# Performance work log

Hardware: AMD Instinct MI355X
Metric: run time of the kernel (lower is better)

## Reference

```python
import jax, jax.numpy as jnp
import numpy as np

COMMITMENT_COST = 0.25


def setup_inputs() -> dict:
    key = jax.random.key(0)
    k1, k2 = jax.random.split(key)
    B, S, D, K = 8, 4096, 256, 1024
    inputs = jax.random.normal(k1, (B, S, D), dtype=jnp.float32)
    attention_mask = jnp.ones((B, S), dtype=jnp.float32)
    codebook = jax.random.normal(k2, (K, D), dtype=jnp.float32)
    return {"inputs": inputs, "attention_mask": attention_mask, "codebook": codebook}


def reference(inputs, attention_mask, codebook):
    # Inference-mode forward of VectorQuantizer (no EMA update / init / revival).
    B, S, D = inputs.shape
    z = inputs.astype(jnp.float32).reshape(-1, D)          # (N, D)
    m = attention_mask.reshape(-1).astype(jnp.float32)     # (N,)

    cb = codebook.astype(jnp.float32)                      # (K, D)
    # squared L2 distances: ||z||^2 - 2 z e^T + ||e||^2
    dist = (jnp.sum(z * z, axis=-1, keepdims=True)
            - 2.0 * jnp.matmul(z, cb.T)
            + jnp.sum(cb * cb, axis=-1)[None, :])          # (N, K)
    idx = jnp.argmin(dist, axis=-1)                        # (N,)
    q = cb[idx]                                            # (N, D) codebook lookup

    n_valid = jnp.sum(m)
    # mse over valid tokens (elementwise mean, matching F.mse_loss on flat_valid)
    diff = z - jax.lax.stop_gradient(q)
    commitment = jnp.sum(m[:, None] * diff * diff) / (n_valid * D)
    vq_loss = COMMITMENT_COST * commitment

    # straight-through estimator; invalid positions zeroed (as in torch scatter)
    q_ste = z + jax.lax.stop_gradient(q - z)
    quantized = (q_ste * m[:, None]).reshape(B, S, D)
    indices = jnp.where(m > 0, idx, 0).reshape(B, S)
    return quantized, vq_loss, indices
```

## Files before the change

kernel.cpp:

```cpp
#include <hip/hip_runtime.h>
#include <cstdint>

typedef short bf16x8 __attribute__((ext_vector_type(8)));
typedef float f32x4  __attribute__((ext_vector_type(4)));

#define TOK    64
#define CH     64
#define NCH    16
#define BUFW   16384
#define MAXC   32

__device__ __forceinline__ unsigned short f2bf(float f) {
  unsigned u = __float_as_uint(f);
  return (unsigned short)((u + 0x7FFFu + ((u >> 16) & 1u)) >> 16);
}
__device__ __forceinline__ uint4 pack8(float4 a, float4 b) {
  uint4 u;
  u.x = (unsigned)f2bf(a.x) | ((unsigned)f2bf(a.y) << 16);
  u.y = (unsigned)f2bf(a.z) | ((unsigned)f2bf(a.w) << 16);
  u.z = (unsigned)f2bf(b.x) | ((unsigned)f2bf(b.y) << 16);
  u.w = (unsigned)f2bf(b.z) | ((unsigned)f2bf(b.w) << 16);
  return u;
}
__device__ __forceinline__ void gload16(const unsigned short* g, unsigned short* l) {
  __builtin_amdgcn_global_load_lds(
      (const __attribute__((address_space(1))) unsigned int*)(const void*)g,
      (__attribute__((address_space(3))) unsigned int*)(void*)l, 16, 0, 0);
}

__global__ __launch_bounds__(256) void vq_prep(const float* __restrict__ cb,
                                               unsigned short* __restrict__ cb_bf,
                                               float* __restrict__ ee,
                                               float* __restrict__ acc2,
                                               int* __restrict__ done_ctr, int K) {
  if (blockIdx.x == 0 && threadIdx.x == 0) {
    acc2[0] = 0.f; acc2[1] = 0.f; *done_ctr = 0;
  }
  int wave = threadIdx.x >> 6, lane = threadIdx.x & 63;
  int k = blockIdx.x * 4 + wave;
  if (k >= K) return;
  float4 v = *reinterpret_cast<const float4*>(cb + (size_t)k * 256 + lane * 4);
  float s = v.x * v.x + v.y * v.y + v.z * v.z + v.w * v.w;
  #pragma unroll
  for (int off = 32; off; off >>= 1) s += __shfl_down(s, off, 64);
  ushort4 b;
  b.x = f2bf(v.x); b.y = f2bf(v.y); b.z = f2bf(v.z); b.w = f2bf(v.w);
  *reinterpret_cast<ushort4*>(cb_bf + (size_t)k * 256 + lane * 4) = b;
  if (lane == 0) ee[k] = s;
}

__global__ __launch_bounds__(256, 2) void vq_main(
    const float* __restrict__ z, const float* __restrict__ cb,
    const unsigned short* __restrict__ cb_bf, const float* __restrict__ ee,
    const float* __restrict__ mask,
    float* __restrict__ out_q, float* __restrict__ out_idx_f,
    float* __restrict__ out_loss, float* __restrict__ acc2,
    int* __restrict__ done_ctr, int nblocks, int K) {
  __shared__ __align__(16) unsigned short sbuf[2 * BUFW];
  __shared__ float ee_lds[1024];
  __shared__ float znorm[TOK];
  __shared__ int   ccnt[TOK];
  __shared__ unsigned umin[TOK];
  __shared__ unsigned short cand[TOK * MAXC];
  __shared__ unsigned short bkbuf[TOK];
  __shared__ float red[8];
  __shared__ bool  last;

  const int t = threadIdx.x;
  const int n0 = blockIdx.x * TOK;
  const int wv = t >> 6, lane = t & 63;
  const int quad = lane >> 4, l15 = lane & 15;
  const int q16 = t & 15;

  ee_lds[t]       = ee[t];
  ee_lds[t + 256] = ee[t + 256];
  ee_lds[t + 512] = ee[t + 512];
  ee_lds[t + 768] = ee[t + 768];
  if (t < TOK) { ccnt[t] = 0; umin[t] = 0x7F7FFFFFu; }

  #pragma unroll
  for (int pass = 0; pass < 4; ++pass) {
    int row = pass * 16 + (t >> 4);
    const float* zr = z + (size_t)(n0 + row) * 256;
    float ssq = 0.f;
    #pragma unroll
    for (int j = 0; j < 2; ++j) {
      float4 a = *reinterpret_cast<const float4*>(zr + q16 * 16 + j * 8);
      float4 b = *reinterpret_cast<const float4*>(zr + q16 * 16 + j * 8 + 4);
      ssq += a.x*a.x + a.y*a.y + a.z*a.z + a.w*a.w
           + b.x*b.x + b.y*b.y + b.z*b.z + b.w*b.w;
      int g = q16 * 2 + j;
      *reinterpret_cast<uint4*>(&sbuf[row * 256 + ((g ^ (row & 7)) * 8)]) = pack8(a, b);
    }
    #pragma unroll
    for (int off = 1; off < 16; off <<= 1) ssq += __shfl_xor(ssq, off, 64);
    if (q16 == 0) znorm[row] = sqrtf(ssq);
  }
  __syncthreads();

  bf16x8 afrag[8];
  float  znreg[4];
  {
    int row = wv * 16 + l15;
    #pragma unroll
    for (int kk = 0; kk < 8; ++kk) {
      int g = (quad + kk * 4) ^ (row & 7);
      afrag[kk] = *reinterpret_cast<const bf16x8*>(&sbuf[row * 256 + g * 8]);
    }
    #pragma unroll
    for (int r = 0; r < 4; ++r)
      znreg[r] = znorm[wv * 16 + quad * 4 + r];
  }
  __syncthreads();

  {
    #pragma unroll
    for (int i = 0; i < 8; ++i) {
      int f = (wv * 8 + i) * 64 + lane;
      int row = f >> 5, slot = f & 31;
      gload16(cb_bf + (size_t)row * 256 + ((slot ^ (row & 7)) * 8),
              &sbuf[(size_t)(wv * 512 + i * 64) * 8]);
    }
  }
  asm volatile("s_waitcnt vmcnt(0)" ::: "memory");
  __syncthreads();

  for (int lc = 0; lc < NCH; ++lc) {
    const int kbase = lc * CH;
    unsigned short* cur = &sbuf[(lc & 1) * BUFW];
    unsigned short* nxt = &sbuf[((lc + 1) & 1) * BUFW];
    if (lc < NCH - 1) {
      const unsigned short* base = cb_bf + (size_t)(kbase + CH) * 256;
      #pragma unroll
      for (int i = 0; i < 8; ++i) {
        int f = (wv * 8 + i) * 64 + lane;
        int row = f >> 5, slot = f & 31;
        gload16(base + (size_t)row * 256 + ((slot ^ (row & 7)) * 8),
                nxt + (size_t)(wv * 512 + i * 64) * 8);
      }
    }

    f32x4 acc[4];
    #pragma unroll
    for (int ct = 0; ct < 4; ++ct) acc[ct] = (f32x4){0.f, 0.f, 0.f, 0.f};
    __builtin_amdgcn_s_setprio(1);
    #pragma unroll
    for (int kk = 0; kk < 8; ++kk) {
      int gx = quad + kk * 4;
      bf16x8 b0 = *reinterpret_cast<const bf16x8*>(&cur[(l15)      * 256 + ((gx ^ ( l15       & 7)) * 8)]);
      bf16x8 b1 = *reinterpret_cast<const bf16x8*>(&cur[(16 + l15) * 256 + ((gx ^ ((16 + l15) & 7)) * 8)]);
      bf16x8 b2 = *reinterpret_cast<const bf16x8*>(&cur[(32 + l15) * 256 + ((gx ^ ((32 + l15) & 7)) * 8)]);
      bf16x8 b3 = *reinterpret_cast<const bf16x8*>(&cur[(48 + l15) * 256 + ((gx ^ ((48 + l15) & 7)) * 8)]);
      acc[0] = __builtin_amdgcn_mfma_f32_16x16x32_bf16(afrag[kk], b0, acc[0], 0, 0, 0);
      acc[1] = __builtin_amdgcn_mfma_f32_16x16x32_bf16(afrag[kk], b1, acc[1], 0, 0, 0);
      acc[2] = __builtin_amdgcn_mfma_f32_16x16x32_bf16(afrag[kk], b2, acc[2], 0, 0, 0);
      acc[3] = __builtin_amdgcn_mfma_f32_16x16x32_bf16(afrag[kk], b3, acc[3], 0, 0, 0);
    }
    __builtin_amdgcn_s_setprio(0);

    float e0 = ee_lds[kbase + l15],      e1 = ee_lds[kbase + 16 + l15];
    float e2 = ee_lds[kbase + 32 + l15], e3 = ee_lds[kbase + 48 + l15];
    float en0 = sqrtf(e0), en1 = sqrtf(e1), en2 = sqrtf(e2), en3 = sqrtf(e3);
    #pragma unroll
    for (int r = 0; r < 4; ++r) {
      float d0 = e0 - 2.f * acc[0][r];
      float d1 = e1 - 2.f * acc[1][r];
      float d2 = e2 - 2.f * acc[2][r];
      float d3 = e3 - 2.f * acc[3][r];
      int tok = wv * 16 + quad * 4 + r;
      float dm = fmaxf(fminf(fminf(d0, d1), fminf(d2, d3)), 0.f);
      atomicMin(&umin[tok], __float_as_uint(dm));
      float am = __uint_as_float(umin[tok]);
      float zn = znreg[r];
      if (d0 <= am + 1.5f + 0.002f * zn * en0) {
        int sl = atomicAdd(&ccnt[tok], 1);
        if (sl < MAXC) cand[tok * MAXC + sl] = (unsigned short)(kbase + l15);
      }
      if (d1 <= am + 1.5f + 0.002f * zn * en1) {
        int sl = atomicAdd(&ccnt[tok], 1);
        if (sl < MAXC) cand[tok * MAXC + sl] = (unsigned short)(kbase + 16 + l15);
      }
      if (d2 <= am + 1.5f + 0.002f * zn * en2) {
        int sl = atomicAdd(&ccnt[tok], 1);
        if (sl < MAXC) cand[tok * MAXC + sl] = (unsigned short)(kbase + 32 + l15);
      }
      if (d3 <= am + 1.5f + 0.002f * zn * en3) {
        int sl = atomicAdd(&ccnt[tok], 1);
        if (sl < MAXC) cand[tok * MAXC + sl] = (unsigned short)(kbase + 48 + l15);
      }
    }
    asm volatile("s_waitcnt vmcnt(0)" ::: "memory");
    __syncthreads();
  }

  for (int it = 0; it < 16; ++it) {
    int tok = wv * 16 + it;
    int n = n0 + tok;
    float4 zv = *reinterpret_cast<const float4*>(z + (size_t)n * 256 + lane * 4);
    int cnt = ccnt[tok];
    float bs = 3.4e38f; int bk = 0;
    if (cnt > MAXC) {
      for (int k = 0; k < K; k += 2) {
        float4 ea = *reinterpret_cast<const float4*>(cb + (size_t)k * 256 + lane * 4);
        float4 eb = *reinterpret_cast<const float4*>(cb + (size_t)(k + 1) * 256 + lane * 4);
        float pa = zv.x * ea.x + zv.y * ea.y + zv.z * ea.z + zv.w * ea.w;
        float pb = zv.x * eb.x + zv.y * eb.y + zv.z * eb.z + zv.w * eb.w;
        #pragma unroll
        for (int off = 32; off; off >>= 1) {
          pa += __shfl_xor(pa, off, 64);
          pb += __shfl_xor(pb, off, 64);
        }
        float sa = ee_lds[k] - 2.f * pa;
        float sb = ee_lds[k + 1] - 2.f * pb;
        if (sa < bs) { bs = sa; bk = k; }
        if (sb < bs) { bs = sb; bk = k + 1; }
      }
    } else {
      int c = 0;
      for (; c + 4 <= cnt; c += 4) {
        int k0 = cand[tok * MAXC + c];
        int k1 = cand[tok * MAXC + c + 1];
        int k2 = cand[tok * MAXC + c + 2];
        int k3 = cand[tok * MAXC + c + 3];
        float4 e0 = *reinterpret_cast<const float4*>(cb + (size_t)k0 * 256 + lane * 4);
        float4 e1 = *reinterpret_cast<const float4*>(cb + (size_t)k1 * 256 + lane * 4);
        float4 e2 = *reinterpret_cast<const float4*>(cb + (size_t)k2 * 256 + lane * 4);
        float4 e3 = *reinterpret_cast<const float4*>(cb + (size_t)k3 * 256 + lane * 4);
        float p0 = zv.x * e0.x + zv.y * e0.y + zv.z * e0.z + zv.w * e0.w;
        float p1 = zv.x * e1.x + zv.y * e1.y + zv.z * e1.z + zv.w * e1.w;
        float p2 = zv.x * e2.x + zv.y * e2.y + zv.z * e2.z + zv.w * e2.w;
        float p3 = zv.x * e3.x + zv.y * e3.y + zv.z * e3.z + zv.w * e3.w;
        #pragma unroll
        for (int off = 32; off; off >>= 1) {
          p0 += __shfl_xor(p0, off, 64);
          p1 += __shfl_xor(p1, off, 64);
          p2 += __shfl_xor(p2, off, 64);
          p3 += __shfl_xor(p3, off, 64);
        }
        float s0 = ee_lds[k0] - 2.f * p0;
        float s1 = ee_lds[k1] - 2.f * p1;
        float s2 = ee_lds[k2] - 2.f * p2;
        float s3 = ee_lds[k3] - 2.f * p3;
        if (s0 < bs || (s0 == bs && k0 < bk)) { bs = s0; bk = k0; }
        if (s1 < bs || (s1 == bs && k1 < bk)) { bs = s1; bk = k1; }
        if (s2 < bs || (s2 == bs && k2 < bk)) { bs = s2; bk = k2; }
        if (s3 < bs || (s3 == bs && k3 < bk)) { bs = s3; bk = k3; }
      }
      for (; c < cnt; ++c) {
        int k = cand[tok * MAXC + c];
        float4 ev = *reinterpret_cast<const float4*>(cb + (size_t)k * 256 + lane * 4);
        float dp = zv.x * ev.x + zv.y * ev.y + zv.z * ev.z + zv.w * ev.w;
        #pragma unroll
        for (int off = 32; off; off >>= 1) dp += __shfl_xor(dp, off, 64);
        float s = ee_lds[k] - 2.f * dp;
        if (s < bs || (s == bs && k < bk)) { bs = s; bk = k; }
      }
    }
    bkbuf[tok] = (unsigned short)bk;
  }

  float lsum = 0.f, msum = 0.f;
  for (int it = 0; it < 16; it += 2) {
    int tokA = wv * 16 + it, tokB = tokA + 1;
    int na = n0 + tokA, nb = n0 + tokB;
    int ba = bkbuf[tokA], bb = bkbuf[tokB];
    float4 za = *reinterpret_cast<const float4*>(z + (size_t)na * 256 + lane * 4);
    float4 zb = *reinterpret_cast<const float4*>(z + (size_t)nb * 256 + lane * 4);
    float4 qa = *reinterpret_cast<const float4*>(cb + (size_t)ba * 256 + lane * 4);
    float4 qb = *reinterpret_cast<const float4*>(cb + (size_t)bb * 256 + lane * 4);
    float ma = mask[na], mb = mask[nb];
    float4 oa; oa.x = qa.x * ma; oa.y = qa.y * ma; oa.z = qa.z * ma; oa.w = qa.w * ma;
    float4 ob; ob.x = qb.x * mb; ob.y = qb.y * mb; ob.z = qb.z * mb; ob.w = qb.w * mb;
    *reinterpret_cast<float4*>(out_q + (size_t)na * 256 + lane * 4) = oa;
    *reinterpret_cast<float4*>(out_q + (size_t)nb * 256 + lane * 4) = ob;
    float dxa = za.x - qa.x, dya = za.y - qa.y, dza = za.z - qa.z, dwa = za.w - qa.w;
    float dxb = zb.x - qb.x, dyb = zb.y - qb.y, dzb = zb.z - qb.z, dwb = zb.w - qb.w;
    lsum = fmaf(ma, dxa * dxa + dya * dya + dza * dza + dwa * dwa, lsum);
    lsum = fmaf(mb, dxb * dxb + dyb * dyb + dzb * dzb + dwb * dwb, lsum);
    if (lane == 0) {
      msum += ma + mb;
      out_idx_f[na] = (ma > 0.f) ? (float)ba : 0.f;
      out_idx_f[nb] = (mb > 0.f) ? (float)bb : 0.f;
    }
  }
  #pragma unroll
  for (int off = 32; off; off >>= 1) lsum += __shfl_down(lsum, off, 64);
  if (lane == 0) { red[wv] = lsum; red[4 + wv] = msum; }
  __syncthreads();
  if (t == 0) {
    atomicAdd(&acc2[0], red[0] + red[1] + red[2] + red[3]);
    atomicAdd(&acc2[1], red[4] + red[5] + red[6] + red[7]);
    __threadfence();
    int prev = atomicAdd(done_ctr, 1);
    last = (prev == nblocks - 1);
  }
  __syncthreads();
  if (last && t == 0) {
    float s  = atomicAdd(&acc2[0], 0.0f);
    float nv = atomicAdd(&acc2[1], 0.0f);
    out_loss[0] = (nv > 0.f) ? (0.25f * s / (nv * 256.0f)) : 0.0f;
  }
}

extern "C" void kernel_launch(void* const* d_in, const int* in_sizes, int n_in,
                              void* d_out, int out_size, void* d_ws, size_t ws_size,
                              hipStream_t stream) {
  const float* z    = (const float*)d_in[0];
  const float* mask = (const float*)d_in[1];
  const float* cb   = (const float*)d_in[2];
  const int N = in_sizes[1];
  const int D = 256;
  const int K = in_sizes[2] / D;

  float* wsf  = (float*)d_ws;
  float* acc2 = wsf;
  int*   dctr = (int*)(wsf + 2);
  float* ee   = wsf + 8;
  unsigned short* cb_bf = (unsigned short*)(ee + K);

  float* out_q     = (float*)d_out;
  float* out_loss  = out_q + (size_t)N * D;
  float* out_idx_f = out_loss + 1;

  vq_prep<<<(K + 3) / 4, 256, 0, stream>>>(cb, cb_bf, ee, acc2, dctr, K);
  vq_main<<<N / TOK, 256, 0, stream>>>(z, cb, cb_bf, ee, mask, out_q,
                                       out_idx_f, out_loss, acc2, dctr, N / TOK, K);
}
```

Baseline: 178.4 us.

## Split codebook across wave pairs with per-wave private double buffers, no block barriers

Restructures the distance GEMM so each wave owns half the tokens (two 16-row A tiles) and half the codebook (512 entries), streaming 16-entry chunks into a private per-wave LDS double buffer. This removes the per-chunk __syncthreads and full vmcnt(0) waits, replacing them with a partial vmcnt wait so loads overlap compute without block-wide synchronization. The trade-off is smaller MFMA batches per chunk (2 instead of 4 per k-step), twice as many chunks, and more frequent atomic min/candidate updates per distance. The per-wave wait relies on each lane seeing its own global_load_lds completions without a barrier, which is a correctness subtlety.

```diff
diff --git a/kernel.cpp b/kernel.cpp
--- a/kernel.cpp
+++ b/kernel.cpp
@@ -5,9 +5,8 @@
 typedef float f32x4  __attribute__((ext_vector_type(4)));
 
 #define TOK    64
-#define CH     64
-#define NCH    16
-#define BUFW   16384
+#define CCH    16
+#define NCH    32
 #define MAXC   32
 
 __device__ __forceinline__ unsigned short f2bf(float f) {
@@ -56,7 +55,7 @@
     float* __restrict__ out_q, float* __restrict__ out_idx_f,
     float* __restrict__ out_loss, float* __restrict__ acc2,
     int* __restrict__ done_ctr, int nblocks, int K) {
-  __shared__ __align__(16) unsigned short sbuf[2 * BUFW];
+  __shared__ __align__(16) unsigned short sbuf[32768];
   __shared__ float ee_lds[1024];
   __shared__ float znorm[TOK];
   __shared__ int   ccnt[TOK];
@@ -69,6 +68,7 @@
   const int t = threadIdx.x;
   const int n0 = blockIdx.x * TOK;
   const int wv = t >> 6, lane = t & 63;
+  const int p = wv & 1, kh = wv >> 1;
   const int quad = lane >> 4, l15 = lane & 15;
   const int q16 = t & 15;
 
@@ -98,100 +98,83 @@
   }
   __syncthreads();
 
-  bf16x8 afrag[8];
-  float  znreg[4];
-  {
-    int row = wv * 16 + l15;
+  bf16x8 afrag[2][8];
+  float  znreg[2][4];
+  #pragma unroll
+  for (int s = 0; s < 2; ++s) {
+    int row = p * 32 + s * 16 + l15;
     #pragma unroll
     for (int kk = 0; kk < 8; ++kk) {
       int g = (quad + kk * 4) ^ (row & 7);
-      afrag[kk] = *reinterpret_cast<const bf16x8*>(&sbuf[row * 256 + g * 8]);
+      afrag[s][kk] = *reinterpret_cast<const bf16x8*>(&sbuf[row * 256 + g * 8]);
     }
     #pragma unroll
     for (int r = 0; r < 4; ++r)
-      znreg[r] = znorm[wv * 16 + quad * 4 + r];
-  }
-  __syncthreads();
-
-  {
-    #pragma unroll
-    for (int i = 0; i < 8; ++i) {
-      int f = (wv * 8 + i) * 64 + lane;
-      int row = f >> 5, slot = f & 31;
-      gload16(cb_bf + (size_t)row * 256 + ((slot ^ (row & 7)) * 8),
-              &sbuf[(size_t)(wv * 512 + i * 64) * 8]);
-    }
-  }
-  asm volatile("s_waitcnt vmcnt(0)" ::: "memory");
-  __syncthreads();
+      znreg[s][r] = znorm[p * 32 + s * 16 + quad * 4 + r];
+  }
+  __syncthreads();
+
+  unsigned short* wbuf = &sbuf[wv * 8192];
+  const unsigned short* cbh = cb_bf + (size_t)kh * 512 * 256;
+
+  #pragma unroll
+  for (int i = 0; i < 8; ++i) {
+    int f = i * 64 + lane;
+    int row = f >> 5, slot = f & 31;
+    gload16(cbh + (size_t)row * 256 + ((slot ^ (row & 7)) * 8),
+            wbuf + (size_t)(i * 64) * 8);
+  }
 
   for (int lc = 0; lc < NCH; ++lc) {
-    const int kbase = lc * CH;
-    unsigned short* cur = &sbuf[(lc & 1) * BUFW];
-    unsigned short* nxt = &sbuf[((lc + 1) & 1) * BUFW];
+    unsigned short* cur = wbuf + (lc & 1) * 4096;
+    unsigned short* nxt = wbuf + ((lc + 1) & 1) * 4096;
     if (lc < NCH - 1) {
-      const unsigned short* base = cb_bf + (size_t)(kbase + CH) * 256;
+      const unsigned short* base = cbh + (size_t)(lc + 1) * CCH * 256;
       #pragma unroll
       for (int i = 0; i < 8; ++i) {
-        int f = (wv * 8 + i) * 64 + lane;
+        int f = i * 64 + lane;
         int row = f >> 5, slot = f & 31;
         gload16(base + (size_t)row * 256 + ((slot ^ (row & 7)) * 8),
-                nxt + (size_t)(wv * 512 + i * 64) * 8);
-      }
-    }
-
-    f32x4 acc[4];
-    #pragma unroll
-    for (int ct = 0; ct < 4; ++ct) acc[ct] = (f32x4){0.f, 0.f, 0.f, 0.f};
+                nxt + (size_t)(i * 64) * 8);
+      }
+      asm volatile("s_waitcnt vmcnt(8)" ::: "memory");
+    } else {
+      asm volatile("s_waitcnt vmcnt(0)" ::: "memory");
+    }
+
+    const int kbase = kh * 512 + lc * CCH;
+    float e0 = ee_lds[kbase + l15];
+
+    f32x4 acc[2];
+    acc[0] = (f32x4){0.f, 0.f, 0.f, 0.f};
+    acc[1] = (f32x4){0.f, 0.f, 0.f, 0.f};
     __builtin_amdgcn_s_setprio(1);
     #pragma unroll
     for (int kk = 0; kk < 8; ++kk) {
-      int gx = quad + kk * 4;
-      bf16x8 b0 = *reinterpret_cast<const bf16x8*>(&cur[(l15)      * 256 + ((gx ^ ( l15       & 7)) * 8)]);
-      bf16x8 b1 = *reinterpret_cast<const bf16x8*>(&cur[(16 + l15) * 256 + ((gx ^ ((16 + l15) & 7)) * 8)]);
-      bf16x8 b2 = *reinterpret_cast<const bf16x8*>(&cur[(32 + l15) * 256 + ((gx ^ ((32 + l15) & 7)) * 8)]);
-      bf16x8 b3 = *reinterpret_cast<const bf16x8*>(&cur[(48 + l15) * 256 + ((gx ^ ((48 + l15) & 7)) * 8)]);
-      acc[0] = __builtin_amdgcn_mfma_f32_16x16x32_bf16(afrag[kk], b0, acc[0], 0, 0, 0);
-      acc[1] = __builtin_amdgcn_mfma_f32_16x16x32_bf16(afrag[kk], b1, acc[1], 0, 0, 0);
-      acc[2] = __builtin_amdgcn_mfma_f32_16x16x32_bf16(afrag[kk], b2, acc[2], 0, 0, 0);
-      acc[3] = __builtin_amdgcn_mfma_f32_16x16x32_bf16(afrag[kk], b3, acc[3], 0, 0, 0);
+      int gph = (quad + kk * 4) ^ (l15 & 7);
+      bf16x8 b = *reinterpret_cast<const bf16x8*>(&cur[l15 * 256 + gph * 8]);
+      acc[0] = __builtin_amdgcn_mfma_f32_16x16x32_bf16(afrag[0][kk], b, acc[0], 0, 0, 0);
+      acc[1] = __builtin_amdgcn_mfma_f32_16x16x32_bf16(afrag[1][kk], b, acc[1], 0, 0, 0);
     }
     __builtin_amdgcn_s_setprio(0);
 
-    float e0 = ee_lds[kbase + l15],      e1 = ee_lds[kbase + 16 + l15];
-    float e2 = ee_lds[kbase + 32 + l15], e3 = ee_lds[kbase + 48 + l15];
-    float en0 = sqrtf(e0), en1 = sqrtf(e1), en2 = sqrtf(e2), en3 = sqrtf(e3);
-    #pragma unroll
-    for (int r = 0; r < 4; ++r) {
-      float d0 = e0 - 2.f * acc[0][r];
-      float d1 = e1 - 2.f * acc[1][r];
-      float d2 = e2 - 2.f * acc[2][r];
-      float d3 = e3 - 2.f * acc[3][r];
-      int tok = wv * 16 + quad * 4 + r;
-      float dm = fmaxf(fminf(fminf(d0, d1), fminf(d2, d3)), 0.f);
-      atomicMin(&umin[tok], __float_as_uint(dm));
-      float am = __uint_as_float(umin[tok]);
-      float zn = znreg[r];
-      if (d0 <= am + 1.5f + 0.002f * zn * en0) {
-        int sl = atomicAdd(&ccnt[tok], 1);
-        if (sl < MAXC) cand[tok * MAXC + sl] = (unsigned short)(kbase + l15);
-      }
-      if (d1 <= am + 1.5f + 0.002f * zn * en1) {
-        int sl = atomicAdd(&ccnt[tok], 1);
-        if (sl < MAXC) cand[tok * MAXC + sl] = (unsigned short)(kbase + 16 + l15);
-      }
-      if (d2 <= am + 1.5f + 0.002f * zn * en2) {
-        int sl = atomicAdd(&ccnt[tok], 1);
-        if (sl < MAXC) cand[tok * MAXC + sl] = (unsigned short)(kbase + 32 + l15);
-      }
-      if (d3 <= am + 1.5f + 0.002f * zn * en3) {
-        int sl = atomicAdd(&ccnt[tok], 1);
-        if (sl < MAXC) cand[tok * MAXC + sl] = (unsigned short)(kbase + 48 + l15);
-      }
-    }
-    asm volatile("s_waitcnt vmcnt(0)" ::: "memory");
-    __syncthreads();
-  }
+    float en0 = sqrtf(e0);
+    #pragma unroll
+    for (int s = 0; s < 2; ++s) {
+      #pragma unroll
+      for (int r = 0; r < 4; ++r) {
+        float d0 = e0 - 2.f * acc[s][r];
+        int tok = p * 32 + s * 16 + quad * 4 + r;
+        atomicMin(&umin[tok], __float_as_uint(fmaxf(d0, 0.f)));
+        float am = __uint_as_float(umin[tok]);
+        if (d0 <= am + 1.5f + 0.002f * znreg[s][r] * en0) {
+          int sl = atomicAdd(&ccnt[tok], 1);
+          if (sl < MAXC) cand[tok * MAXC + sl] = (unsigned short)(kbase + l15);
+        }
+      }
+    }
+  }
+  __syncthreads();
 
   for (int it = 0; it < 16; ++it) {
     int tok = wv * 16 + it;
```

Measured after the change: 216.7 us. 21.4% more time.

## Store approximate distances with candidates and skip fp32 rescoring when one survives

Applied to the files above, without the earlier changes.

Each candidate slot now packs the truncated bf16 MFMA distance together with the code index. After the coarse pass, a wave-wide ballot re-filters the candidates against the final per-token minimum, using a threshold built from the global max codebook norm. When exactly one candidate survives, its index is taken directly and the fp32 codebook reads and dot-product reductions are skipped. This adds a block-wide max reduction of the codebook norms and doubles the LDS footprint of the candidate buffer. Correctness now depends on the error bound holding with the coarser global norm.

```diff
diff --git a/kernel.cpp b/kernel.cpp
--- a/kernel.cpp
+++ b/kernel.cpp
@@ -61,7 +61,7 @@
   __shared__ float znorm[TOK];
   __shared__ int   ccnt[TOK];
   __shared__ unsigned umin[TOK];
-  __shared__ unsigned short cand[TOK * MAXC];
+  __shared__ unsigned cand[TOK * MAXC];
   __shared__ unsigned short bkbuf[TOK];
   __shared__ float red[8];
   __shared__ bool  last;
@@ -72,11 +72,13 @@
   const int quad = lane >> 4, l15 = lane & 15;
   const int q16 = t & 15;
 
-  ee_lds[t]       = ee[t];
-  ee_lds[t + 256] = ee[t + 256];
-  ee_lds[t + 512] = ee[t + 512];
-  ee_lds[t + 768] = ee[t + 768];
+  float ea = ee[t], eb = ee[t + 256], ec = ee[t + 512], ed = ee[t + 768];
+  ee_lds[t] = ea; ee_lds[t + 256] = eb; ee_lds[t + 512] = ec; ee_lds[t + 768] = ed;
   if (t < TOK) { ccnt[t] = 0; umin[t] = 0x7F7FFFFFu; }
+  float em = fmaxf(fmaxf(ea, eb), fmaxf(ec, ed));
+  #pragma unroll
+  for (int off = 32; off; off >>= 1) em = fmaxf(em, __shfl_xor(em, off, 64));
+  if (lane == 0) red[wv] = em;
 
   #pragma unroll
   for (int pass = 0; pass < 4; ++pass) {
@@ -97,6 +99,8 @@
     if (q16 == 0) znorm[row] = sqrtf(ssq);
   }
   __syncthreads();
+
+  const float enmax = sqrtf(fmaxf(fmaxf(red[0], red[1]), fmaxf(red[2], red[3])));
 
   bf16x8 afrag[8];
   float  znreg[4];
@@ -174,19 +178,23 @@
       float zn = znreg[r];
       if (d0 <= am + 1.5f + 0.002f * zn * en0) {
         int sl = atomicAdd(&ccnt[tok], 1);
-        if (sl < MAXC) cand[tok * MAXC + sl] = (unsigned short)(kbase + l15);
+        if (sl < MAXC) cand[tok * MAXC + sl] =
+            (__float_as_uint(fmaxf(d0, 0.f)) & 0xFFFFFC00u) | (unsigned)(kbase + l15);
       }
       if (d1 <= am + 1.5f + 0.002f * zn * en1) {
         int sl = atomicAdd(&ccnt[tok], 1);
-        if (sl < MAXC) cand[tok * MAXC + sl] = (unsigned short)(kbase + 16 + l15);
+        if (sl < MAXC) cand[tok * MAXC + sl] =
+            (__float_as_uint(fmaxf(d1, 0.f)) & 0xFFFFFC00u) | (unsigned)(kbase + 16 + l15);
       }
       if (d2 <= am + 1.5f + 0.002f * zn * en2) {
         int sl = atomicAdd(&ccnt[tok], 1);
-        if (sl < MAXC) cand[tok * MAXC + sl] = (unsigned short)(kbase + 32 + l15);
+        if (sl < MAXC) cand[tok * MAXC + sl] =
+            (__float_as_uint(fmaxf(d2, 0.f)) & 0xFFFFFC00u) | (unsigned)(kbase + 32 + l15);
       }
       if (d3 <= am + 1.5f + 0.002f * zn * en3) {
         int sl = atomicAdd(&ccnt[tok], 1);
-        if (sl < MAXC) cand[tok * MAXC + sl] = (unsigned short)(kbase + 48 + l15);
+        if (sl < MAXC) cand[tok * MAXC + sl] =
+            (__float_as_uint(fmaxf(d3, 0.f)) & 0xFFFFFC00u) | (unsigned)(kbase + 48 + l15);
       }
     }
     asm volatile("s_waitcnt vmcnt(0)" ::: "memory");
@@ -196,15 +204,16 @@
   for (int it = 0; it < 16; ++it) {
     int tok = wv * 16 + it;
     int n = n0 + tok;
-    float4 zv = *reinterpret_cast<const float4*>(z + (size_t)n * 256 + lane * 4);
     int cnt = ccnt[tok];
-    float bs = 3.4e38f; int bk = 0;
+    int bk = 0;
     if (cnt > MAXC) {
+      float4 zv = *reinterpret_cast<const float4*>(z + (size_t)n * 256 + lane * 4);
+      float bs = 3.4e38f;
       for (int k = 0; k < K; k += 2) {
-        float4 ea = *reinterpret_cast<const float4*>(cb + (size_t)k * 256 + lane * 4);
-        float4 eb = *reinterpret_cast<const float4*>(cb + (size_t)(k + 1) * 256 + lane * 4);
-        float pa = zv.x * ea.x + zv.y * ea.y + zv.z * ea.z + zv.w * ea.w;
-        float pb = zv.x * eb.x + zv.y * eb.y + zv.z * eb.z + zv.w * eb.w;
+        float4 ca = *reinterpret_cast<const float4*>(cb + (size_t)k * 256 + lane * 4);
+        float4 cbv = *reinterpret_cast<const float4*>(cb + (size_t)(k + 1) * 256 + lane * 4);
+        float pa = zv.x * ca.x + zv.y * ca.y + zv.z * ca.z + zv.w * ca.w;
+        float pb = zv.x * cbv.x + zv.y * cbv.y + zv.z * cbv.z + zv.w * cbv.w;
         #pragma unroll
         for (int off = 32; off; off >>= 1) {
           pa += __shfl_xor(pa, off, 64);
@@ -216,44 +225,56 @@
         if (sb < bs) { bs = sb; bk = k + 1; }
       }
     } else {
-      int c = 0;
-      for (; c + 4 <= cnt; c += 4) {
-        int k0 = cand[tok * MAXC + c];
-        int k1 = cand[tok * MAXC + c + 1];
-        int k2 = cand[tok * MAXC + c + 2];
-        int k3 = cand[tok * MAXC + c + 3];
-        float4 e0 = *reinterpret_cast<const float4*>(cb + (size_t)k0 * 256 + lane * 4);
-        float4 e1 = *reinterpret_cast<const float4*>(cb + (size_t)k1 * 256 + lane * 4);
-        float4 e2 = *reinterpret_cast<const float4*>(cb + (size_t)k2 * 256 + lane * 4);
-        float4 e3 = *reinterpret_cast<const float4*>(cb + (size_t)k3 * 256 + lane * 4);
-        float p0 = zv.x * e0.x + zv.y * e0.y + zv.z * e0.z + zv.w * e0.w;
-        float p1 = zv.x * e1.x + zv.y * e1.y + zv.z * e1.z + zv.w * e1.w;
-        float p2 = zv.x * e2.x + zv.y * e2.y + zv.z * e2.z + zv.w * e2.w;
-        float p3 = zv.x * e3.x + zv.y * e3.y + zv.z * e3.z + zv.w * e3.w;
-        #pragma unroll
-        for (int off = 32; off; off >>= 1) {
-          p0 += __shfl_xor(p0, off, 64);
-          p1 += __shfl_xor(p1, off, 64);
-          p2 += __shfl_xor(p2, off, 64);
-          p3 += __shfl_xor(p3, off, 64);
+      float thr = __uint_as_float(umin[tok]) + 1.5f + 0.002f * znorm[tok] * enmax;
+      int c = (lane < cnt) ? lane : 0;
+      unsigned pe = cand[tok * MAXC + c];
+      bool flag = (lane < cnt) && (__uint_as_float(pe & 0xFFFFFC00u) <= thr);
+      unsigned long long msk = __ballot(flag);
+      if (__popcll(msk) == 1) {
+        int cc = __ffsll((long long)msk) - 1;
+        bk = (int)(cand[tok * MAXC + cc] & 1023u);
+      } else {
+        float4 zv = *reinterpret_cast<const float4*>(z + (size_t)n * 256 + lane * 4);
+        float bs = 3.4e38f; bk = 1 << 29;
+        int cc = 0;
+        for (; cc + 4 <= cnt; cc += 4) {
+          int k0 = cand[tok * MAXC + cc]     & 1023;
+          int k1 = cand[tok * MAXC + cc + 1] & 1023;
+          int k2 = cand[tok * MAXC + cc + 2] & 1023;
+          int k3 = cand[tok * MAXC + cc + 3] & 1023;
+          float4 e0 = *reinterpret_cast<const float4*>(cb + (size_t)k0 * 256 + lane * 4);
+          float4 e1 = *reinterpret_cast<const float4*>(cb + (size_t)k1 * 256 + lane * 4);
+          float4 e2 = *reinterpret_cast<const float4*>(cb + (size_t)k2 * 256 + lane * 4);
+          float4 e3 = *reinterpret_cast<const float4*>(cb + (size_t)k3 * 256 + lane * 4);
+          float p0 = zv.x * e0.x + zv.y * e0.y + zv.z * e0.z + zv.w * e0.w;
+          float p1 = zv.x * e1.x + zv.y * e1.y + zv.z * e1.z + zv.w * e1.w;
+          float p2 = zv.x * e2.x + zv.y * e2.y + zv.z * e2.z + zv.w * e2.w;
+          float p3 = zv.x * e3.x + zv.y * e3.y + zv.z * e3.z + zv.w * e3.w;
+          #pragma unroll
+          for (int off = 32; off; off >>= 1) {
+            p0 += __shfl_xor(p0, off, 64);
+            p1 += __shfl_xor(p1, off, 64);
+            p2 += __shfl_xor(p2, off, 64);
+            p3 += __shfl_xor(p3, off, 64);
+          }
+          float s0 = ee_lds[k0] - 2.f * p0;
+          float s1 = ee_lds[k1] - 2.f * p1;
+          float s2 = ee_lds[k2] - 2.f * p2;
+          float s3 = ee_lds[k3] - 2.f * p3;
+          if (s0 < bs || (s0 == bs && k0 < bk)) { bs = s0; bk = k0; }
+          if (s1 < bs || (s1 == bs && k1 < bk)) { bs = s1; bk = k1; }
+          if (s2 < bs || (s2 == bs && k2 < bk)) { bs = s2; bk = k2; }
+          if (s3 < bs || (s3 == bs && k3 < bk)) { bs = s3; bk = k3; }
         }
-        float s0 = ee_lds[k0] - 2.f * p0;
-        float s1 = ee_lds[k1] - 2.f * p1;
-        float s2 = ee_lds[k2] - 2.f * p2;
-        float s3 = ee_lds[k3] - 2.f * p3;
-        if (s0 < bs || (s0 == bs && k0 < bk)) { bs = s0; bk = k0; }
-        if (s1 < bs || (s1 == bs && k1 < bk)) { bs = s1; bk = k1; }
-        if (s2 < bs || (s2 == bs && k2 < bk)) { bs = s2; bk = k2; }
-        if (s3 < bs || (s3 == bs && k3 < bk)) { bs = s3; bk = k3; }
-      }
-      for (; c < cnt; ++c) {
-        int k = cand[tok * MAXC + c];
-        float4 ev = *reinterpret_cast<const float4*>(cb + (size_t)k * 256 + lane * 4);
-        float dp = zv.x * ev.x + zv.y * ev.y + zv.z * ev.z + zv.w * ev.w;
-        #pragma unroll
-        for (int off = 32; off; off >>= 1) dp += __shfl_xor(dp, off, 64);
-        float s = ee_lds[k] - 2.f * dp;
-        if (s < bs || (s == bs && k < bk)) { bs = s; bk = k; }
+        for (; cc < cnt; ++cc) {
+          int k = cand[tok * MAXC + cc] & 1023;
+          float4 ev = *reinterpret_cast<const float4*>(cb + (size_t)k * 256 + lane * 4);
+          float dp = zv.x * ev.x + zv.y * ev.y + zv.z * ev.z + zv.w * ev.w;
+          #pragma unroll
+          for (int off = 32; off; off >>= 1) dp += __shfl_xor(dp, off, 64);
+          float s = ee_lds[k] - 2.f * dp;
+          if (s < bs || (s == bs && k < bk)) { bs = s; bk = k; }
+        }
       }
     }
     bkbuf[tok] = (unsigned short)bk;
```

Result: faster. 165.0 us (-7.5%).
